# Kernel optimization log

Measured on AMD Instinct MI355X. Metric: run time of the kernel, lower is better.

Reference implementation:

```python
import jax, jax.numpy as jnp
import numpy as np

B, C, H, W = 64, 512, 8, 8
K = 100            # num_class
H1, HID, L = 64, 128, 32   # ae_hidden[0], fixed hidd, ae_latent
CLIP = 100.0       # CSSRClassifier.clip_len
RED = -0.1         # model='pcssr' -> -1, times gamma=0.1
PUSH_THRESH = 10000.0


def setup_inputs() -> dict:
    key = jax.random.key(0)
    ks = jax.random.split(key, 9)
    s = lambda fan_in: 1.0 / np.sqrt(fan_in)  # kaiming-ish 1x1 conv init scale
    return {
        "x": jax.random.normal(ks[0], (B, C, H, W), jnp.float32),
        "ycls": jax.random.randint(ks[1], (B,), 0, K),
        "safe_margin_all": jax.random.normal(ks[2], (K,), jnp.float32),
        "safe_distance_all": jax.random.normal(ks[3], (K,), jnp.float32),
        "W1": jax.random.normal(ks[4], (K, H1, C), jnp.float32) * s(C),
        "W2": jax.random.normal(ks[5], (K, HID, H1), jnp.float32) * s(H1),
        "W3": jax.random.normal(ks[6], (K, L, HID), jnp.float32) * s(HID),
        "prototypes": jax.random.normal(ks[7], (K, L, H, W), jnp.float32),
        "prototypes1": jax.random.normal(ks[8], (K, L, H, W), jnp.float32),
    }


def reference(x, ycls, safe_margin_all, safe_distance_all, W1, W2, W3, prototypes, prototypes1):
    P = H * W
    xf = x.reshape(B, C, P)
    # per-class 1x1-conv encoder (tanh after every conv), batched over classes k
    h = jnp.tanh(jnp.einsum('koc,bcp->kbop', W1, xf))      # [K,B,H1,P]
    h = jnp.tanh(jnp.einsum('koi,kbip->kbop', W2, h))      # [K,B,HID,P]
    lt = jnp.tanh(jnp.einsum('koi,kbip->kbop', W3, h))     # [K,B,L,P]
    p = prototypes.reshape(K, 1, L, P)
    p1 = prototypes1.reshape(K, 1, L, P)
    # squared-L2 distance over channel dim, scaled by reduction, clipped
    er = jnp.clip(jnp.sum((lt - p) ** 2, axis=2) * RED, -CLIP, CLIP)    # [K,B,P]
    er1 = jnp.clip(jnp.sum((lt - p1) ** 2, axis=2) * RED, -CLIP, CLIP)  # [K,B,P]
    # training losses (pull on er1, push on er), vectorized across classes
    f = jnp.sum(er, axis=2)    # [K,B] spatial-summed errors
    f1 = jnp.sum(er1, axis=2)  # [K,B]
    cls_ids = jnp.arange(K)[:, None]
    mask_eq = (ycls[None, :] == cls_ids).astype(f.dtype)   # [K,B]
    n_eq = jnp.sum(mask_eq, axis=1)
    pull = jnp.sum(jnp.where(n_eq > 0,
                             jnp.sum(f1 * mask_eq, axis=1) / jnp.maximum(n_eq, 1.0),
                             0.0))
    comb = (1.0 - mask_eq) * (f < PUSH_THRESH).astype(f.dtype)
    n_comb = jnp.sum(comb, axis=1)
    push = jnp.sum(jnp.where(n_comb > 0,
                             jnp.sum(f * comb, axis=1) / jnp.maximum(n_comb, 1.0),
                             0.0))
    # cat per-class [B,1,H,W] errors along dim 1 -> [B,K,H,W]
    logits = jnp.transpose(er, (1, 0, 2)).reshape(B, K, H, W)
    logits1 = jnp.transpose(er1, (1, 0, 2)).reshape(B, K, H, W)
    return logits, logits1, pull, push
```

## Files before the change

kernel.cpp:

```cpp
#include <hip/hip_runtime.h>

typedef short  s16x8  __attribute__((ext_vector_type(8)));
typedef float  f32x16 __attribute__((ext_vector_type(16)));
typedef unsigned short u16;
typedef unsigned int   u32;

#define MFMA32(a,b,c) __builtin_amdgcn_mfma_f32_32x32x16_bf16((a),(b),(c),0,0,0)
#define KCLS 100
#define VMCNT(n) asm volatile("s_waitcnt vmcnt(" #n ")" ::: "memory")
#define BAR()    __builtin_amdgcn_s_barrier()

__device__ __forceinline__ u16 f2bf(float f) {
  return (u16)(__builtin_bit_cast(unsigned, f) >> 16);
}

__device__ __forceinline__ u32 pk2bf(float lo, float hi) {
#if __has_builtin(__builtin_amdgcn_perm)
  return __builtin_amdgcn_perm(__builtin_bit_cast(u32, hi),
                               __builtin_bit_cast(u32, lo), 0x07060302u);
#else
  return (__builtin_bit_cast(u32, lo) >> 16) | (__builtin_bit_cast(u32, hi) & 0xffff0000u);
#endif
}

__device__ __forceinline__ float tanh_fast(float x) {
  float e = __builtin_amdgcn_exp2f(x * 2.8853900817779268f);
  return 1.0f - 2.0f * __builtin_amdgcn_rcpf(e + 1.0f);
}

__device__ __forceinline__ void ld_lds16(const void* g, void* l) {
  __builtin_amdgcn_global_load_lds(
      (const __attribute__((address_space(1))) unsigned char*)g,
      (__attribute__((address_space(3))) unsigned char*)l, 16, 0, 0);
}

__global__ void prep(const float* __restrict__ x, const float* __restrict__ w1,
                     const float* __restrict__ w2, const float* __restrict__ w3,
                     u16* __restrict__ xF, u16* __restrict__ W1F,
                     u16* __restrict__ W2F, u16* __restrict__ W3F,
                     float* __restrict__ fz, float* __restrict__ out2) {
  __shared__ float tile[64][65];
  const int bid = blockIdx.x, t = threadIdx.x;
  if (bid == 0 && t < 2) out2[t] = 0.f;
  if (bid < 512) {
    const int b = bid >> 3, ck = bid & 7;
    #pragma unroll
    for (int j = 0; j < 4; j++) {
      int e4 = j * 1024 + t * 4;
      int c = e4 >> 6, p0 = e4 & 63;
      float4 v = *(const float4*)(x + ((size_t)b * 512 + ck * 64 + c) * 64 + p0);
      tile[c][p0] = v.x; tile[c][p0 + 1] = v.y; tile[c][p0 + 2] = v.z; tile[c][p0 + 3] = v.w;
    }
    __syncthreads();
    #pragma unroll
    for (int i = 0; i < 2; i++) {
      int s = i * 256 + t;
      int ksl = s >> 7, ph = (s >> 6) & 1, lane = s & 63;
      int cb = ksl * 16 + (lane >> 5) * 8, pp = ph * 32 + (lane & 31);
      u16 o[8];
      #pragma unroll
      for (int jj = 0; jj < 8; jj++) o[jj] = f2bf(tile[cb + jj][pp]);
      *(uint4*)(xF + (((size_t)b * 64 + (ck * 4 + ksl) * 2 + ph) * 512) + lane * 8) = *(uint4*)o;
    }
  } else if (bid < 1312) {
    const int wb = bid - 512, k = wb >> 3, ct = wb & 7;
    #pragma unroll
    for (int j = 0; j < 4; j++) {
      int e4 = j * 1024 + t * 4;
      int r = e4 >> 6, c = e4 & 63;
      float4 v = *(const float4*)(w1 + ((size_t)k * 64 + r) * 512 + ct * 64 + c);
      tile[r][c] = v.x; tile[r][c + 1] = v.y; tile[r][c + 2] = v.z; tile[r][c + 3] = v.w;
    }
    __syncthreads();
    #pragma unroll
    for (int i = 0; i < 2; i++) {
      int s = i * 256 + t;
      int frl = s >> 6, lane = s & 63;
      int m = (frl & 1) * 32 + (lane & 31);
      int cl = (frl >> 1) * 16 + (lane >> 5) * 8;
      u16 o[8];
      #pragma unroll
      for (int jj = 0; jj < 8; jj++) o[jj] = f2bf(tile[m][cl + jj]);
      *(uint4*)(W1F + ((size_t)(k * 64 + ct * 8 + frl) * 512) + lane * 8) = *(uint4*)o;
    }
  } else if (bid < 1512) {
    const int wb = bid - 1312, k = wb >> 1, mt = wb & 1;
    #pragma unroll
    for (int j = 0; j < 4; j++) {
      int e4 = j * 1024 + t * 4;
      int r = e4 >> 6, c = e4 & 63;
      float4 v = *(const float4*)(w2 + ((size_t)k * 128 + mt * 64 + r) * 64 + c);
      tile[r][c] = v.x; tile[r][c + 1] = v.y; tile[r][c + 2] = v.z; tile[r][c + 3] = v.w;
    }
    __syncthreads();
    #pragma unroll
    for (int i = 0; i < 2; i++) {
      int s = i * 256 + t;
      int frl = s >> 6, lane = s & 63;
      int kb = frl >> 1, m4l = frl & 1;
      int ml = m4l * 32 + (lane & 31);
      int cl = kb * 16 + (lane >> 5) * 8;
      u16 o[8];
      #pragma unroll
      for (int jj = 0; jj < 8; jj++) o[jj] = f2bf(tile[ml][cl + jj]);
      *(uint4*)(W2F + ((size_t)(k * 16 + kb * 4 + mt * 2 + m4l) * 512) + lane * 8) = *(uint4*)o;
    }
  } else if (bid < 1612) {
    const int k = bid - 1512;
    #pragma unroll
    for (int j = 0; j < 4; j++) {
      int e4 = j * 1024 + t * 4;
      int r = e4 >> 7, c = e4 & 127;
      float4 v = *(const float4*)(w3 + ((size_t)k * 32 + r) * 128 + c);
      int rr = r + ((c >> 6) << 5), cc = c & 63;
      tile[rr][cc] = v.x; tile[rr][cc + 1] = v.y; tile[rr][cc + 2] = v.z; tile[rr][cc + 3] = v.w;
    }
    __syncthreads();
    #pragma unroll
    for (int i = 0; i < 2; i++) {
      int s = i * 256 + t;
      int frl = s >> 6, lane = s & 63;
      int m = lane & 31;
      int c0 = frl * 16 + (lane >> 5) * 8;
      int rr = m + ((c0 >> 6) << 5), cc = c0 & 63;
      u16 o[8];
      #pragma unroll
      for (int jj = 0; jj < 8; jj++) o[jj] = f2bf(tile[rr][cc + jj]);
      *(uint4*)(W3F + ((size_t)(k * 8 + frl) * 512) + lane * 8) = *(uint4*)o;
    }
  } else {
    int i4 = (bid - 1612) * 256 + t;
    if (i4 < 3200) {
      float4 z = {0.f, 0.f, 0.f, 0.f};
      *(float4*)(fz + (size_t)i4 * 4) = z;
    }
  }
}

template<int GG>
__device__ __forceinline__ s16x8 mk_bfrag(const f32x16 a) {
  u32 P0 = pk2bf(tanh_fast(a[8 * GG + 0]), tanh_fast(a[8 * GG + 1]));
  u32 P1 = pk2bf(tanh_fast(a[8 * GG + 2]), tanh_fast(a[8 * GG + 3]));
  u32 Q0 = pk2bf(tanh_fast(a[8 * GG + 4]), tanh_fast(a[8 * GG + 5]));
  u32 Q1 = pk2bf(tanh_fast(a[8 * GG + 6]), tanh_fast(a[8 * GG + 7]));
  asm("v_permlane32_swap_b32 %0, %1" : "+v"(P0), "+v"(Q0));
  asm("v_permlane32_swap_b32 %0, %1" : "+v"(P1), "+v"(Q1));
  int4 wv = { (int)P0, (int)P1, (int)Q0, (int)Q1 };
  return __builtin_bit_cast(s16x8, wv);
}

__global__ __launch_bounds__(256, 4) void cssr_main(
    const u16* __restrict__ W1F, const u16* __restrict__ W2F, const u16* __restrict__ W3F,
    const u16* __restrict__ xF, const float* __restrict__ protos,
    const float* __restrict__ protos1, float* __restrict__ out,
    float* __restrict__ fw, float* __restrict__ f1w)
{
  __shared__ u16 pool[20480];
  const int bid = blockIdx.x;
  const int k = bid >> 5, bpair = bid & 31;
  const int tid = threadIdx.x, w = tid >> 6, lane = tid & 63;
  const int bq = w >> 1, ph = w & 1;
  const int b = bpair * 2 + bq;
  const int h = lane >> 5, nn = lane & 31;

  const u16* xw  = xF  + ((size_t)b * 64) * 512 + lane * 8;
  const u16* w1w = W1F + ((size_t)k * 64) * 512 + lane * 8;

  s16x8 Bc[4], Bn[4];
  #pragma unroll
  for (int ksl = 0; ksl < 4; ksl++)
    Bc[ksl] = *(const s16x8*)(xw + (ksl * 2 + ph) * 512);
  ld_lds16(w1w + (w * 2 + 0) * 512, &pool[(2 * w + 0) * 512]);
  ld_lds16(w1w + (w * 2 + 1) * 512, &pool[(2 * w + 1) * 512]);

  f32x16 acc1[2] = {};
  #pragma unroll
  for (int ci = 0; ci < 8; ci++) {
    const int cb = ci & 1;
    if (ci < 7) {
      #pragma unroll
      for (int ksl = 0; ksl < 4; ksl++)
        Bn[ksl] = *(const s16x8*)(xw + (((ci + 1) * 4 + ksl) * 2 + ph) * 512);
      ld_lds16(w1w + (((ci + 1) * 4 + w) * 2 + 0) * 512, &pool[(cb ^ 1) * 4096 + (2 * w + 0) * 512]);
      ld_lds16(w1w + (((ci + 1) * 4 + w) * 2 + 1) * 512, &pool[(cb ^ 1) * 4096 + (2 * w + 1) * 512]);
      if (ci == 6) {
        #pragma unroll
        for (int j = 0; j < 4; j++)
          ld_lds16(W2F + ((size_t)k * 16 + w * 4 + j) * 512 + lane * 8,
                   &pool[8192 + (w * 4 + j) * 512]);
        ld_lds16(W3F + ((size_t)k * 8 + w * 2 + 0) * 512 + lane * 8, &pool[16384 + (w * 2 + 0) * 512]);
        ld_lds16(W3F + ((size_t)k * 8 + w * 2 + 1) * 512 + lane * 8, &pool[16384 + (w * 2 + 1) * 512]);
      }
    }
    if (ci == 6) { VMCNT(12); } else { VMCNT(6); }
    BAR();
    #pragma unroll
    for (int ksl = 0; ksl < 4; ksl++) {
      s16x8 A0 = *(const s16x8*)&pool[cb * 4096 + (ksl * 2 + 0) * 512 + lane * 8];
      s16x8 A1 = *(const s16x8*)&pool[cb * 4096 + (ksl * 2 + 1) * 512 + lane * 8];
      acc1[0] = MFMA32(A0, Bc[ksl], acc1[0]);
      acc1[1] = MFMA32(A1, Bc[ksl], acc1[1]);
    }
    if (ci < 7) {
      #pragma unroll
      for (int ksl = 0; ksl < 4; ksl++) Bc[ksl] = Bn[ksl];
      BAR();
    }
  }

  s16x8 b1[4];
  b1[0] = mk_bfrag<0>(acc1[0]); b1[1] = mk_bfrag<1>(acc1[0]);
  b1[2] = mk_bfrag<0>(acc1[1]); b1[3] = mk_bfrag<1>(acc1[1]);

  VMCNT(2); BAR();

  f32x16 acc2[4] = {};
  __builtin_amdgcn_s_setprio(1);
  #pragma unroll
  for (int kb = 0; kb < 4; kb++) {
    #pragma unroll
    for (int m4 = 0; m4 < 4; m4++) {
      s16x8 A = *(const s16x8*)&pool[8192 + (kb * 4 + m4) * 512 + lane * 8];
      acc2[m4] = MFMA32(A, b1[kb], acc2[m4]);
    }
  }
  __builtin_amdgcn_s_setprio(0);

  VMCNT(0); BAR();

  const int p = ph * 32 + nn;
  const float* pr  = protos  + (size_t)k * 2048 + p;
  const float* pr1 = protos1 + (size_t)k * 2048 + p;
  float prv[16], pr1v[16];
  #pragma unroll
  for (int g = 0; g < 4; g++) {
    #pragma unroll
    for (int q = 0; q < 4; q++) {
      int m = q + 8 * g + 4 * h;
      prv [g * 4 + q] = pr [m * 64];
      pr1v[g * 4 + q] = pr1[m * 64];
    }
  }

  s16x8 b2[8];
  b2[0] = mk_bfrag<0>(acc2[0]); b2[1] = mk_bfrag<1>(acc2[0]);
  b2[2] = mk_bfrag<0>(acc2[1]); b2[3] = mk_bfrag<1>(acc2[1]);
  b2[4] = mk_bfrag<0>(acc2[2]); b2[5] = mk_bfrag<1>(acc2[2]);
  b2[6] = mk_bfrag<0>(acc2[3]); b2[7] = mk_bfrag<1>(acc2[3]);

  f32x16 acc3 = {};
  __builtin_amdgcn_s_setprio(1);
  #pragma unroll
  for (int kb = 0; kb < 8; kb++) {
    s16x8 A = *(const s16x8*)&pool[16384 + kb * 512 + lane * 8];
    acc3 = MFMA32(A, b2[kb], acc3);
  }
  __builtin_amdgcn_s_setprio(0);

  float d2 = 0.f, d21 = 0.f;
  #pragma unroll
  for (int g = 0; g < 4; g++) {
    #pragma unroll
    for (int q = 0; q < 4; q++) {
      float lt = tanh_fast(acc3[g * 4 + q]);
      float d = lt - prv [g * 4 + q];  d2  += d * d;
      float e = lt - pr1v[g * 4 + q];  d21 += e * e;
    }
  }
  d2 += __shfl_xor(d2, 32); d21 += __shfl_xor(d21, 32);
  float er  = fminf(fmaxf(d2  * -0.1f, -100.f), 100.f);
  float er1 = fminf(fmaxf(d21 * -0.1f, -100.f), 100.f);
  if (h == 0) {
    out[(size_t)b * 6400 + k * 64 + p]          = er;
    out[409600 + (size_t)b * 6400 + k * 64 + p] = er1;
  }
  float s = er, s1 = er1;
  s += __shfl_xor(s, 1);  s1 += __shfl_xor(s1, 1);
  s += __shfl_xor(s, 2);  s1 += __shfl_xor(s1, 2);
  s += __shfl_xor(s, 4);  s1 += __shfl_xor(s1, 4);
  s += __shfl_xor(s, 8);  s1 += __shfl_xor(s1, 8);
  s += __shfl_xor(s, 16); s1 += __shfl_xor(s1, 16);
  if (lane == 0) {
    atomicAdd(&fw [k * 64 + b], s);
    atomicAdd(&f1w[k * 64 + b], s1);
  }
}

__global__ void finalize(const float* __restrict__ f, const float* __restrict__ f1,
                         const int* __restrict__ ycls, float* __restrict__ out2) {
  const int k = blockIdx.x, b = threadIdx.x;
  float fv = f[k * 64 + b], f1v = f1[k * 64 + b];
  bool eq = (ycls[b] == k);
  bool cb = (!eq) && (fv < 10000.f);
  float s1 = eq ? f1v : 0.f, ne = eq ? 1.f : 0.f;
  float s  = cb ? fv  : 0.f, nc = cb ? 1.f : 0.f;
  #pragma unroll
  for (int o = 1; o < 64; o <<= 1) {
    s1 += __shfl_xor(s1, o); ne += __shfl_xor(ne, o);
    s  += __shfl_xor(s,  o); nc += __shfl_xor(nc, o);
  }
  if (b == 0) {
    if (ne > 0.f) atomicAdd(&out2[0], s1 / ne);
    if (nc > 0.f) atomicAdd(&out2[1], s / nc);
  }
}

extern "C" void kernel_launch(void* const* d_in, const int* in_sizes, int n_in,
                              void* d_out, int out_size, void* d_ws, size_t ws_size,
                              hipStream_t stream) {
  const float* x     = (const float*)d_in[0];
  const int*   ycls  = (const int*)d_in[1];
  const float* W1    = (const float*)d_in[4];
  const float* W2    = (const float*)d_in[5];
  const float* W3    = (const float*)d_in[6];
  const float* prot  = (const float*)d_in[7];
  const float* prot1 = (const float*)d_in[8];
  float* out = (float*)d_out;

  char* ws = (char*)d_ws;
  u16*  xFb = (u16*)(ws);
  u16*  W1F = (u16*)(ws + 4194304);
  u16*  W2F = (u16*)(ws + 10747904);
  u16*  W3F = (u16*)(ws + 12386304);
  float* fw  = (float*)(ws + 13205504);
  float* f1w = (float*)(ws + 13231104);
  float* out2 = out + 819200;

  prep<<<1625, 256, 0, stream>>>(x, W1, W2, W3, xFb, W1F, W2F, W3F, fw, out2);
  cssr_main<<<KCLS * 32, 256, 0, stream>>>(W1F, W2F, W3F, xFb, prot, prot1,
                                           out, fw, f1w);
  finalize<<<KCLS, 64, 0, stream>>>(fw, f1w, ycls, out2);
}
```

Before: 142.7 us.

## Shrink LDS pool by streaming W2 in two halves to raise occupancy

Reorders the packed W2 fragment layout so each half of the hidden outputs is contiguous. The main kernel then loads W2 into LDS in two halves, overwriting the first half after it is consumed. This reduces shared memory from 40KB to 32KB per block and raises launch bounds to 5 blocks per CU. It also computes layer 2 one 32-row tile at a time, which lowers accumulator register pressure. The cost is an extra barrier and a serialized global-to-LDS load in the middle of the kernel.

```diff
diff --git a/kernel.cpp b/kernel.cpp
--- a/kernel.cpp
+++ b/kernel.cpp
@@ -103,7 +103,7 @@
       u16 o[8];
       #pragma unroll
       for (int jj = 0; jj < 8; jj++) o[jj] = f2bf(tile[ml][cl + jj]);
-      *(uint4*)(W2F + ((size_t)(k * 16 + kb * 4 + mt * 2 + m4l) * 512) + lane * 8) = *(uint4*)o;
+      *(uint4*)(W2F + ((size_t)(k * 16 + (mt * 2 + m4l) * 4 + kb) * 512) + lane * 8) = *(uint4*)o;
     }
   } else if (bid < 1612) {
     const int k = bid - 1512;
@@ -149,13 +149,13 @@
   return __builtin_bit_cast(s16x8, wv);
 }
 
-__global__ __launch_bounds__(256, 4) void cssr_main(
+__global__ __launch_bounds__(256, 5) void cssr_main(
     const u16* __restrict__ W1F, const u16* __restrict__ W2F, const u16* __restrict__ W3F,
     const u16* __restrict__ xF, const float* __restrict__ protos,
     const float* __restrict__ protos1, float* __restrict__ out,
     float* __restrict__ fw, float* __restrict__ f1w)
 {
-  __shared__ u16 pool[20480];
+  __shared__ u16 pool[16384];
   const int bid = blockIdx.x;
   const int k = bid >> 5, bpair = bid & 31;
   const int tid = threadIdx.x, w = tid >> 6, lane = tid & 63;
@@ -165,6 +165,8 @@
 
   const u16* xw  = xF  + ((size_t)b * 64) * 512 + lane * 8;
   const u16* w1w = W1F + ((size_t)k * 64) * 512 + lane * 8;
+  const u16* w2w = W2F + ((size_t)k * 16) * 512 + lane * 8;
+  const u16* w3w = W3F + ((size_t)k * 8)  * 512 + lane * 8;
 
   s16x8 Bc[4], Bn[4];
   #pragma unroll
@@ -184,15 +186,15 @@
       ld_lds16(w1w + (((ci + 1) * 4 + w) * 2 + 0) * 512, &pool[(cb ^ 1) * 4096 + (2 * w + 0) * 512]);
       ld_lds16(w1w + (((ci + 1) * 4 + w) * 2 + 1) * 512, &pool[(cb ^ 1) * 4096 + (2 * w + 1) * 512]);
       if (ci == 6) {
-        #pragma unroll
-        for (int j = 0; j < 4; j++)
-          ld_lds16(W2F + ((size_t)k * 16 + w * 4 + j) * 512 + lane * 8,
-                   &pool[8192 + (w * 4 + j) * 512]);
-        ld_lds16(W3F + ((size_t)k * 8 + w * 2 + 0) * 512 + lane * 8, &pool[16384 + (w * 2 + 0) * 512]);
-        ld_lds16(W3F + ((size_t)k * 8 + w * 2 + 1) * 512 + lane * 8, &pool[16384 + (w * 2 + 1) * 512]);
+        ld_lds16(w2w + (w * 2 + 0) * 512, &pool[8192 + (w * 2 + 0) * 512]);
+        ld_lds16(w2w + (w * 2 + 1) * 512, &pool[8192 + (w * 2 + 1) * 512]);
+        ld_lds16(w3w + (w * 2 + 0) * 512, &pool[12288 + (w * 2 + 0) * 512]);
+        ld_lds16(w3w + (w * 2 + 1) * 512, &pool[12288 + (w * 2 + 1) * 512]);
       }
     }
-    if (ci == 6) { VMCNT(12); } else { VMCNT(6); }
+    if (ci == 6)      { VMCNT(10); }
+    else if (ci == 7) { VMCNT(4);  }
+    else              { VMCNT(6);  }
     BAR();
     #pragma unroll
     for (int ksl = 0; ksl < 4; ksl++) {
@@ -214,19 +216,39 @@
 
   VMCNT(2); BAR();
 
-  f32x16 acc2[4] = {};
-  __builtin_amdgcn_s_setprio(1);
-  #pragma unroll
-  for (int kb = 0; kb < 4; kb++) {
-    #pragma unroll
-    for (int m4 = 0; m4 < 4; m4++) {
-      s16x8 A = *(const s16x8*)&pool[8192 + (kb * 4 + m4) * 512 + lane * 8];
-      acc2[m4] = MFMA32(A, b1[kb], acc2[m4]);
-    }
-  }
-  __builtin_amdgcn_s_setprio(0);
-
+  s16x8 b2[8];
+  #pragma unroll
+  for (int m4l = 0; m4l < 2; m4l++) {
+    f32x16 a2 = {};
+    __builtin_amdgcn_s_setprio(1);
+    #pragma unroll
+    for (int kb = 0; kb < 4; kb++) {
+      s16x8 A = *(const s16x8*)&pool[8192 + (m4l * 4 + kb) * 512 + lane * 8];
+      a2 = MFMA32(A, b1[kb], a2);
+    }
+    __builtin_amdgcn_s_setprio(0);
+    b2[m4l * 2 + 0] = mk_bfrag<0>(a2);
+    b2[m4l * 2 + 1] = mk_bfrag<1>(a2);
+  }
+
+  BAR();
+  ld_lds16(w2w + (8 + w * 2 + 0) * 512, &pool[8192 + (w * 2 + 0) * 512]);
+  ld_lds16(w2w + (8 + w * 2 + 1) * 512, &pool[8192 + (w * 2 + 1) * 512]);
   VMCNT(0); BAR();
+
+  #pragma unroll
+  for (int m4l = 0; m4l < 2; m4l++) {
+    f32x16 a2 = {};
+    __builtin_amdgcn_s_setprio(1);
+    #pragma unroll
+    for (int kb = 0; kb < 4; kb++) {
+      s16x8 A = *(const s16x8*)&pool[8192 + (m4l * 4 + kb) * 512 + lane * 8];
+      a2 = MFMA32(A, b1[kb], a2);
+    }
+    __builtin_amdgcn_s_setprio(0);
+    b2[4 + m4l * 2 + 0] = mk_bfrag<0>(a2);
+    b2[4 + m4l * 2 + 1] = mk_bfrag<1>(a2);
+  }
 
   const int p = ph * 32 + nn;
   const float* pr  = protos  + (size_t)k * 2048 + p;
@@ -242,17 +264,11 @@
     }
   }
 
-  s16x8 b2[8];
-  b2[0] = mk_bfrag<0>(acc2[0]); b2[1] = mk_bfrag<1>(acc2[0]);
-  b2[2] = mk_bfrag<0>(acc2[1]); b2[3] = mk_bfrag<1>(acc2[1]);
-  b2[4] = mk_bfrag<0>(acc2[2]); b2[5] = mk_bfrag<1>(acc2[2]);
-  b2[6] = mk_bfrag<0>(acc2[3]); b2[7] = mk_bfrag<1>(acc2[3]);
-
   f32x16 acc3 = {};
   __builtin_amdgcn_s_setprio(1);
   #pragma unroll
   for (int kb = 0; kb < 8; kb++) {
-    s16x8 A = *(const s16x8*)&pool[16384 + kb * 512 + lane * 8];
+    s16x8 A = *(const s16x8*)&pool[12288 + kb * 512 + lane * 8];
     acc3 = MFMA32(A, b2[kb], acc3);
   }
   __builtin_amdgcn_s_setprio(0);
```

After: 143.1 us. About the same (+0.3%).
